# Kernel optimization log

Hardware: AMD Instinct MI355X
Metric: run time of the kernel (lower is better)

The kernel has to match this reference:

```python
import jax, jax.numpy as jnp
import numpy as np

B, T, H, O = 2048, 256, 256, 10


def setup_inputs() -> dict:
    key = jax.random.key(0)
    ks = jax.random.split(key, 7)
    # small scales keep gate pre-activations out of saturation
    return {
        "x": jax.random.normal(ks[0], (B, T), jnp.float32),
        "Wx": jax.random.normal(ks[1], (4, H), jnp.float32) * 0.2,   # Linear(1,H) weights, gates g,i,f,o
        "bx": jax.random.normal(ks[2], (4, H), jnp.float32) * 0.1,
        "Wh": jax.random.normal(ks[3], (4, H, H), jnp.float32) * (0.5 / np.sqrt(H)),
        "bh": jax.random.normal(ks[4], (4, H), jnp.float32) * 0.1,
        "W_ph": jax.random.normal(ks[5], (O, H), jnp.float32) * (1.0 / np.sqrt(H)),
        "b_ph": jax.random.normal(ks[6], (O,), jnp.float32) * 0.1,
    }


def reference(x, Wx, bx, Wh, bh, W_ph, b_ph):
    # x: [B, T]; gates stacked on axis 0 in order (g, i, f, o)
    def step(carry, xt):
        h, c = carry  # [B, H] each
        # z[b, g, :] = xt[b] * Wx[g] + bx[g] + h[b] @ Wh[g].T + bh[g]
        z = (xt[:, None, None] * Wx[None] + bx[None]
             + jnp.einsum('bk,gik->bgi', h, Wh) + bh[None])  # [B, 4, H]
        g = jnp.tanh(z[:, 0])
        i = jax.nn.sigmoid(z[:, 1])
        f = jax.nn.sigmoid(z[:, 2])
        o = jax.nn.sigmoid(z[:, 3])
        c = g * i + c * f
        h = jnp.tanh(c) * o
        return (h, c), None

    h0 = jnp.zeros((x.shape[0], Wh.shape[-1]), x.dtype)
    c0 = jnp.zeros_like(h0)
    (h, _), _ = jax.lax.scan(step, (h0, c0), jnp.swapaxes(x, 0, 1))  # scan over T
    return h @ W_ph.T + b_ph  # [B, O]
```

## Files before the change

kernel.cpp:

```cpp
#include <hip/hip_runtime.h>
#include <hip/hip_bf16.h>

typedef int  i32x4 __attribute__((ext_vector_type(4)));
typedef unsigned long long ull;

#define LSTM_T 256
#define LSTM_O 10
#define BTILE 8
#define NBLK 256
#define THREADS 512
#define XSTRIDE 260

#define WS_WQ 0
#define WS_DQ (256 * 1024)

__device__ __forceinline__ float sigmoid_f(float x) {
    return __builtin_amdgcn_rcpf(1.0f + __expf(-x));
}
__device__ __forceinline__ float tanh_f(float x) {
    return fmaf(2.0f, __builtin_amdgcn_rcpf(1.0f + __expf(-2.0f * x)), -1.0f);
}

#define LDS_BARRIER() asm volatile("s_waitcnt lgkmcnt(0)\n\ts_barrier" ::: "memory")

__global__ void __launch_bounds__(64) quant_wh_kernel(const float* __restrict__ Wh,
                                                      char* __restrict__ Wq,
                                                      float* __restrict__ dq) {
    const int row  = blockIdx.x;
    const int lane = threadIdx.x;
    float4 v = *(const float4*)(Wh + (size_t)row * 256 + lane * 4);
    float m = fmaxf(fmaxf(fabsf(v.x), fabsf(v.y)), fmaxf(fabsf(v.z), fabsf(v.w)));
#pragma unroll
    for (int off = 32; off; off >>= 1) m = fmaxf(m, __shfl_xor(m, off));
    m = fmaxf(m, 1e-20f);
    float s = 127.f / m;
    int q0 = (int)rintf(v.x * s), q1 = (int)rintf(v.y * s);
    int q2 = (int)rintf(v.z * s), q3 = (int)rintf(v.w * s);
    unsigned int pk = (unsigned)(q0 & 255) | ((unsigned)(q1 & 255) << 8) |
                      ((unsigned)(q2 & 255) << 16) | ((unsigned)(q3 & 255) << 24);
    ((unsigned int*)Wq)[row * 64 + lane] = pk;
    if (lane == 0) dq[row] = m / 16129.f;
}

__global__ void __launch_bounds__(THREADS, 2) lstm_kernel(
    const float* __restrict__ x,
    const float* __restrict__ Wx,
    const float* __restrict__ bx,
    const float* __restrict__ bh,
    const char*  __restrict__ Wq,
    const float* __restrict__ dq,
    const float* __restrict__ W_ph,
    const float* __restrict__ b_ph,
    float* __restrict__ out)
{
    __shared__ __align__(16) char  h_q[2][8 * 256];
    __shared__ __align__(16) float x_sh[8 * XSTRIDE];

    const int tid   = threadIdx.x;
    const int wave  = tid >> 6;
    const int lane  = tid & 63;
    const int n     = lane & 15;
    const int grp   = lane >> 4;
    const int b0    = blockIdx.x * BTILE;
    const int wcol0 = wave * 32;
    const int tlo   = grp >> 1;
    const int rbase = (grp & 1) * 4;
    const int mycol = wcol0 + tlo * 16 + n;

#pragma unroll
    for (int i = 0; i < 4; ++i) {
        int d = tid + i * 512;
        int row = d >> 8, col = d & 255;
        x_sh[row * XSTRIDE + col] = x[(size_t)(b0 + row) * 256 + col];
    }
    if (tid < 256) ((ull*)h_q[0])[tid] = 0ull;

    i32x4 bW[2][4][4];
#pragma unroll
    for (int tl = 0; tl < 2; ++tl)
#pragma unroll
        for (int g = 0; g < 4; ++g)
#pragma unroll
            for (int ks = 0; ks < 4; ++ks) {
                int col = wcol0 + tl * 16 + n;
                bW[tl][g][ks] = *(const i32x4*)(Wq + (size_t)(g * 256 + col) * 256
                                                + ks * 64 + grp * 16);
                asm volatile("" : "+v"(bW[tl][g][ks]));
            }

    float wxv[4], biv[4], dqv[4];
#pragma unroll
    for (int g = 0; g < 4; ++g) {
        wxv[g] = Wx[g * 256 + mycol];
        biv[g] = bx[g * 256 + mycol] + bh[g * 256 + mycol];
        dqv[g] = dq[g * 256 + mycol];
    }

    float c_st[4] = {0.f, 0.f, 0.f, 0.f};
    float hval[4];
    __syncthreads();

    for (int t = 0; t < LSTM_T; ++t) {
        const char* hb = h_q[t & 1];

        i32x4 aF[4];
#pragma unroll
        for (int ks = 0; ks < 4; ++ks) {
            int r8   = n & 7;
            int addr = ((r8 * 256 + ks * 64 + grp * 16)) ^ (r8 << 5);
            aF[ks] = *(const i32x4*)(hb + addr);
        }

        i32x4 acc[2][4];
#pragma unroll
        for (int tl = 0; tl < 2; ++tl)
#pragma unroll
            for (int g = 0; g < 4; ++g) acc[tl][g] = (i32x4){0, 0, 0, 0};
#pragma unroll
        for (int tl = 0; tl < 2; ++tl)
#pragma unroll
            for (int g = 0; g < 4; ++g)
#pragma unroll
                for (int ks = 0; ks < 4; ++ks)
                    acc[tl][g] = __builtin_amdgcn_mfma_i32_16x16x64_i8(
                        aF[ks], bW[tl][g][ks], acc[tl][g], 0, 0, 0);

#pragma unroll
        for (int q = 0; q < 4; ++q) {
            int r = rbase + q;
            float xt = x_sh[r * XSTRIDE + t];
            float a0 = (float)(tlo ? acc[1][0][q] : acc[0][0][q]);
            float a1 = (float)(tlo ? acc[1][1][q] : acc[0][1][q]);
            float a2 = (float)(tlo ? acc[1][2][q] : acc[0][2][q]);
            float a3 = (float)(tlo ? acc[1][3][q] : acc[0][3][q]);
            float z0 = fmaf(a0, dqv[0], fmaf(xt, wxv[0], biv[0]));
            float z1 = fmaf(a1, dqv[1], fmaf(xt, wxv[1], biv[1]));
            float z2 = fmaf(a2, dqv[2], fmaf(xt, wxv[2], biv[2]));
            float z3 = fmaf(a3, dqv[3], fmaf(xt, wxv[3], biv[3]));
            float gg = tanh_f(z0);
            float ii = sigmoid_f(z1);
            float ff = sigmoid_f(z2);
            float oo = sigmoid_f(z3);
            float cn = fmaf(gg, ii, c_st[q] * ff);
            c_st[q] = cn;
            hval[q] = tanh_f(cn) * oo;
        }

        if (t < LSTM_T - 1) {
            char* hbn = h_q[(t + 1) & 1];
#pragma unroll
            for (int q = 0; q < 4; ++q) {
                int r = rbase + q;
                int hq8 = (int)rintf(hval[q] * 127.f);
                hbn[(r * 256 + mycol) ^ (r << 5)] = (char)hq8;
            }
            LDS_BARRIER();
        } else {
            LDS_BARRIER();
#pragma unroll
            for (int q = 0; q < 4; ++q)
                x_sh[(rbase + q) * XSTRIDE + mycol] = hval[q];
            LDS_BARRIER();
        }
    }

    if (tid < 8 * LSTM_O) {
        int r = tid & 7;
        int o = tid >> 3;
        const float* wrow = W_ph + o * 256;
        const float* hrow = x_sh + r * XSTRIDE;
        float s = 0.f;
#pragma unroll 4
        for (int k0 = 0; k0 < 256; ++k0) {
            int k = (k0 + r * 32) & 255;
            s += hrow[k] * wrow[k];
        }
        out[(size_t)(b0 + r) * LSTM_O + o] = s + b_ph[o];
    }
}

extern "C" void kernel_launch(void* const* d_in, const int* in_sizes, int n_in,
                              void* d_out, int out_size, void* d_ws, size_t ws_size,
                              hipStream_t stream) {
    const float* x    = (const float*)d_in[0];
    const float* Wx   = (const float*)d_in[1];
    const float* bx   = (const float*)d_in[2];
    const float* Wh   = (const float*)d_in[3];
    const float* bh   = (const float*)d_in[4];
    const float* W_ph = (const float*)d_in[5];
    const float* b_ph = (const float*)d_in[6];
    float* out = (float*)d_out;
    char* ws   = (char*)d_ws;

    quant_wh_kernel<<<1024, 64, 0, stream>>>(Wh, ws + WS_WQ, (float*)(ws + WS_DQ));
    lstm_kernel<<<NBLK, THREADS, 0, stream>>>(x, Wx, bx, bh, ws + WS_WQ,
                                              (const float*)(ws + WS_DQ), W_ph, b_ph, out);
}
```

Baseline: 376.5 us.

## Double LSTM block width to 16 waves, one 16-column tile per wave

Raises the block from 512 to 1024 threads so each wave owns a single 16-column tile of the hidden state instead of two. Per-wave MFMA work and register-resident weight fragments are halved, which shortens the serial per-timestep critical path. Each lane now handles two batch rows rather than four in the gate epilogue. The cost is a 16-wave barrier each step and a launch-bounds change from 2 to 4 that tightens the register budget.

Measured after the change: 368.6 us. 1.02x faster.

```diff
diff --git a/kernel.cpp b/kernel.cpp
--- a/kernel.cpp
+++ b/kernel.cpp
@@ -8,7 +8,7 @@
 #define LSTM_O 10
 #define BTILE 8
 #define NBLK 256
-#define THREADS 512
+#define THREADS 1024
 #define XSTRIDE 260
 
 #define WS_WQ 0
@@ -42,7 +42,7 @@
     if (lane == 0) dq[row] = m / 16129.f;
 }
 
-__global__ void __launch_bounds__(THREADS, 2) lstm_kernel(
+__global__ void __launch_bounds__(THREADS, 4) lstm_kernel(
     const float* __restrict__ x,
     const float* __restrict__ Wx,
     const float* __restrict__ bx,
@@ -62,31 +62,27 @@
     const int n     = lane & 15;
     const int grp   = lane >> 4;
     const int b0    = blockIdx.x * BTILE;
-    const int wcol0 = wave * 32;
-    const int tlo   = grp >> 1;
-    const int rbase = (grp & 1) * 4;
-    const int mycol = wcol0 + tlo * 16 + n;
+    const int hi    = grp >> 1;
+    const int rbase = (grp & 1) * 4 + hi * 2;
+    const int mycol = wave * 16 + n;
 
 #pragma unroll
-    for (int i = 0; i < 4; ++i) {
-        int d = tid + i * 512;
+    for (int i = 0; i < 2; ++i) {
+        int d = tid + i * 1024;
         int row = d >> 8, col = d & 255;
         x_sh[row * XSTRIDE + col] = x[(size_t)(b0 + row) * 256 + col];
     }
     if (tid < 256) ((ull*)h_q[0])[tid] = 0ull;
 
-    i32x4 bW[2][4][4];
+    i32x4 bW[4][4];
 #pragma unroll
-    for (int tl = 0; tl < 2; ++tl)
+    for (int g = 0; g < 4; ++g)
 #pragma unroll
-        for (int g = 0; g < 4; ++g)
-#pragma unroll
-            for (int ks = 0; ks < 4; ++ks) {
-                int col = wcol0 + tl * 16 + n;
-                bW[tl][g][ks] = *(const i32x4*)(Wq + (size_t)(g * 256 + col) * 256
-                                                + ks * 64 + grp * 16);
-                asm volatile("" : "+v"(bW[tl][g][ks]));
-            }
+        for (int ks = 0; ks < 4; ++ks) {
+            bW[g][ks] = *(const i32x4*)(Wq + (size_t)(g * 256 + mycol) * 256
+                                        + ks * 64 + grp * 16);
+            asm volatile("" : "+v"(bW[g][ks]));
+        }
 
     float wxv[4], biv[4], dqv[4];
 #pragma unroll
@@ -96,8 +92,8 @@
         dqv[g] = dq[g * 256 + mycol];
     }
 
-    float c_st[4] = {0.f, 0.f, 0.f, 0.f};
-    float hval[4];
+    float c_st[2] = {0.f, 0.f};
+    float hval[2];
     __syncthreads();
 
     for (int t = 0; t < LSTM_T; ++t) {
@@ -107,59 +103,55 @@
 #pragma unroll
         for (int ks = 0; ks < 4; ++ks) {
             int r8   = n & 7;
-            int addr = ((r8 * 256 + ks * 64 + grp * 16)) ^ (r8 << 5);
+            int addr = (r8 * 256 + ks * 64 + grp * 16) ^ (r8 << 5);
             aF[ks] = *(const i32x4*)(hb + addr);
         }
 
-        i32x4 acc[2][4];
+        i32x4 acc[4];
 #pragma unroll
-        for (int tl = 0; tl < 2; ++tl)
+        for (int g = 0; g < 4; ++g) acc[g] = (i32x4){0, 0, 0, 0};
 #pragma unroll
-            for (int g = 0; g < 4; ++g) acc[tl][g] = (i32x4){0, 0, 0, 0};
+        for (int g = 0; g < 4; ++g)
 #pragma unroll
-        for (int tl = 0; tl < 2; ++tl)
-#pragma unroll
-            for (int g = 0; g < 4; ++g)
-#pragma unroll
-                for (int ks = 0; ks < 4; ++ks)
-                    acc[tl][g] = __builtin_amdgcn_mfma_i32_16x16x64_i8(
-                        aF[ks], bW[tl][g][ks], acc[tl][g], 0, 0, 0);
+            for (int ks = 0; ks < 4; ++ks)
+                acc[g] = __builtin_amdgcn_mfma_i32_16x16x64_i8(
+                    aF[ks], bW[g][ks], acc[g], 0, 0, 0);
 
 #pragma unroll
-        for (int q = 0; q < 4; ++q) {
-            int r = rbase + q;
+        for (int qq = 0; qq < 2; ++qq) {
+            int r = rbase + qq;
             float xt = x_sh[r * XSTRIDE + t];
-            float a0 = (float)(tlo ? acc[1][0][q] : acc[0][0][q]);
-            float a1 = (float)(tlo ? acc[1][1][q] : acc[0][1][q]);
-            float a2 = (float)(tlo ? acc[1][2][q] : acc[0][2][q]);
-            float a3 = (float)(tlo ? acc[1][3][q] : acc[0][3][q]);
-            float z0 = fmaf(a0, dqv[0], fmaf(xt, wxv[0], biv[0]));
-            float z1 = fmaf(a1, dqv[1], fmaf(xt, wxv[1], biv[1]));
-            float z2 = fmaf(a2, dqv[2], fmaf(xt, wxv[2], biv[2]));
-            float z3 = fmaf(a3, dqv[3], fmaf(xt, wxv[3], biv[3]));
+            int a0i = hi ? acc[0][qq + 2] : acc[0][qq];
+            int a1i = hi ? acc[1][qq + 2] : acc[1][qq];
+            int a2i = hi ? acc[2][qq + 2] : acc[2][qq];
+            int a3i = hi ? acc[3][qq + 2] : acc[3][qq];
+            float z0 = fmaf((float)a0i, dqv[0], fmaf(xt, wxv[0], biv[0]));
+            float z1 = fmaf((float)a1i, dqv[1], fmaf(xt, wxv[1], biv[1]));
+            float z2 = fmaf((float)a2i, dqv[2], fmaf(xt, wxv[2], biv[2]));
+            float z3 = fmaf((float)a3i, dqv[3], fmaf(xt, wxv[3], biv[3]));
             float gg = tanh_f(z0);
             float ii = sigmoid_f(z1);
             float ff = sigmoid_f(z2);
             float oo = sigmoid_f(z3);
-            float cn = fmaf(gg, ii, c_st[q] * ff);
-            c_st[q] = cn;
-            hval[q] = tanh_f(cn) * oo;
+            float cn = fmaf(gg, ii, c_st[qq] * ff);
+            c_st[qq] = cn;
+            hval[qq] = tanh_f(cn) * oo;
         }
 
         if (t < LSTM_T - 1) {
             char* hbn = h_q[(t + 1) & 1];
 #pragma unroll
-            for (int q = 0; q < 4; ++q) {
-                int r = rbase + q;
-                int hq8 = (int)rintf(hval[q] * 127.f);
+            for (int qq = 0; qq < 2; ++qq) {
+                int r = rbase + qq;
+                int hq8 = (int)rintf(hval[qq] * 127.f);
                 hbn[(r * 256 + mycol) ^ (r << 5)] = (char)hq8;
             }
             LDS_BARRIER();
         } else {
             LDS_BARRIER();
 #pragma unroll
-            for (int q = 0; q < 4; ++q)
-                x_sh[(rbase + q) * XSTRIDE + mycol] = hval[q];
+            for (int qq = 0; qq < 2; ++qq)
+                x_sh[(rbase + qq) * XSTRIDE + mycol] = hval[qq];
             LDS_BARRIER();
         }
     }
```
